# Optimization experiments

Measured on AMD Instinct MI355X. Metric: run time of the kernel, lower is better.

## Reference

```python
import jax, jax.numpy as jnp
import numpy as np
from jax import lax

B = 16
IMG = 384
P = 16
C = 3
DIM = 256
DEPTH = 6
HEADS = 4
DH = 64
INNER = HEADS * DH  # 256
MLP = 512
NC = 21
HP = IMG // P       # 24
N = HP * HP         # 576
PD = C * P * P      # 768
K = 16
SCALE = DH ** -0.5
NEG = -1e9


def _ln(x, g, b):
    mu = x.mean(-1, keepdims=True)
    var = ((x - mu) ** 2).mean(-1, keepdims=True)
    return (x - mu) / jnp.sqrt(var + 1e-5) * g + b


def _conv(x, w, b):
    y = lax.conv_general_dilated(x, w, (1, 1), 'SAME',
                                 dimension_numbers=('NCHW', 'OIHW', 'NCHW'))
    return y + b[None, :, None, None]


def _up2(x):
    b, c, h, w = x.shape
    return jax.image.resize(x, (b, c, 2 * h, 2 * w), 'bilinear')


def _attn(x, g, bt, qkv_w, out_w, out_b, alpha):
    xn = _ln(x, g, bt)
    qkv = xn @ qkv_w                              # [B,N,3*INNER]
    q, k, v = jnp.split(qkv, 3, axis=-1)
    def heads(t):
        return t.reshape(B, N, HEADS, DH).transpose(0, 2, 1, 3)  # b h n d
    q, k, v = heads(q), heads(k), heads(v)
    dots = jnp.einsum('bhid,bhjd->bhij', q, k) * SCALE           # [B,H,N,N]
    vals, idx = lax.top_k(dots, K)                               # [B,H,N,K]
    bi = jnp.arange(B)[:, None, None, None]
    hi = jnp.arange(HEADS)[None, :, None, None]
    ni = jnp.arange(N)[None, None, :, None]
    sparse = jnp.full(dots.shape, NEG, dots.dtype).at[bi, hi, ni, idx].set(vals)
    sparse_attn = jax.nn.softmax(sparse, axis=-1)
    global_attn = jax.nn.softmax(dots, axis=-1)
    a = jnp.clip(alpha, 0.0, 1.0)
    attn = (1 - a) * sparse_attn + a * global_attn
    out = jnp.einsum('bhij,bhjd->bhid', attn, v)                 # [B,H,N,DH]
    out = out.transpose(0, 2, 1, 3).reshape(B, N, INNER)
    return out @ out_w + out_b


def _forward(img, patch_w, patch_b, pos_emb,
             ln1_g, ln1_b, qkv_w, out_w, out_b, alpha,
             ln2_g, ln2_b, ff_w1, ff_b1, ff_w2, ff_b2,
             lnf_g, lnf_b,
             conv1_w, conv1_b, conv2_w, conv2_b, conv3_w, conv3_b):
    # patchify: b c (h p1) (w p2) -> b (h w) (p1 p2 c)
    x = img.reshape(B, C, HP, P, HP, P).transpose(0, 2, 4, 3, 5, 1).reshape(B, N, PD)
    x = x @ patch_w + patch_b + pos_emb
    for i in range(DEPTH):
        x = x + _attn(x, ln1_g[i], ln1_b[i], qkv_w[i], out_w[i], out_b[i], alpha[i])
        h = _ln(x, ln2_g[i], ln2_b[i])
        h = jax.nn.gelu(h @ ff_w1[i] + ff_b1[i], approximate=False)
        x = x + h @ ff_w2[i] + ff_b2[i]
    x = _ln(x, lnf_g, lnf_b)
    x = x.transpose(0, 2, 1).reshape(B, DIM, HP, HP)             # b d h w
    x = jax.nn.relu(_conv(x, conv1_w, conv1_b))
    x = _up2(x)
    x = jax.nn.relu(_conv(x, conv2_w, conv2_b))
    x = _up2(x)
    x = _conv(x, conv3_w, conv3_b)
    return jax.image.resize(x, (B, NC, IMG, IMG), 'bilinear')


def setup_inputs() -> dict:
    key = jax.random.key(0)
    ks = jax.random.split(key, 16)
    s = 0.02
    d = {
        'img': jax.random.normal(ks[0], (B, C, IMG, IMG), jnp.float32),
        'patch_w': jax.random.normal(ks[1], (PD, DIM)) * s,
        'patch_b': jnp.zeros((DIM,)),
        'pos_emb': jax.random.normal(ks[2], (1, N, DIM)) * s,
        'ln1_g': jnp.ones((DEPTH, DIM)), 'ln1_b': jnp.zeros((DEPTH, DIM)),
        'qkv_w': jax.random.normal(ks[3], (DEPTH, DIM, 3 * INNER)) * s,
        'out_w': jax.random.normal(ks[4], (DEPTH, INNER, DIM)) * s,
        'out_b': jnp.zeros((DEPTH, DIM)),
        'alpha': jnp.full((DEPTH,), 0.2),
        'ln2_g': jnp.ones((DEPTH, DIM)), 'ln2_b': jnp.zeros((DEPTH, DIM)),
        'ff_w1': jax.random.normal(ks[5], (DEPTH, DIM, MLP)) * s,
        'ff_b1': jnp.zeros((DEPTH, MLP)),
        'ff_w2': jax.random.normal(ks[6], (DEPTH, MLP, DIM)) * s,
        'ff_b2': jnp.zeros((DEPTH, DIM)),
        'lnf_g': jnp.ones((DIM,)), 'lnf_b': jnp.zeros((DIM,)),
        'conv1_w': jax.random.normal(ks[7], (DIM // 2, DIM, 3, 3)) * s,
        'conv1_b': jnp.zeros((DIM // 2,)),
        'conv2_w': jax.random.normal(ks[8], (DIM // 4, DIM // 2, 3, 3)) * s,
        'conv2_b': jnp.zeros((DIM // 4,)),
        'conv3_w': jax.random.normal(ks[9], (NC, DIM // 4, 1, 1)) * s,
        'conv3_b': jnp.zeros((NC,)),
    }
    return d


def reference(img, patch_w, patch_b, pos_emb,
              ln1_g, ln1_b, qkv_w, out_w, out_b, alpha,
              ln2_g, ln2_b, ff_w1, ff_b1, ff_w2, ff_b2,
              lnf_g, lnf_b,
              conv1_w, conv1_b, conv2_w, conv2_b, conv3_w, conv3_b):
    return _forward(img, patch_w, patch_b, pos_emb,
                    ln1_g, ln1_b, qkv_w, out_w, out_b, alpha,
                    ln2_g, ln2_b, ff_w1, ff_b1, ff_w2, ff_b2,
                    lnf_g, lnf_b,
                    conv1_w, conv1_b, conv2_w, conv2_b, conv3_w, conv3_b)
```

## Files before the change

kernel.cpp:

```cpp
#include <hip/hip_runtime.h>
#include <cfloat>
#include <cmath>

constexpr int NB    = 16;
constexpr int IMGSZ = 384;
constexpr int PSZ   = 16;
constexpr int NCH   = 3;
constexpr int DMODEL= 256;
constexpr int DEPTH = 6;
constexpr int NHEAD = 4;
constexpr int DHEAD = 64;
constexpr int DQKV  = 768;
constexpr int QKS   = 512;
constexpr int DMLP  = 512;
constexpr int NCLS  = 21;
constexpr int HPATCH= 24;
constexpr int NTOK  = 576;
constexpr int NPD   = 768;
constexpr int TOPK  = 16;
constexpr int NROWS = NB * NTOK;
constexpr int OUT_TOTAL = NB * NCLS * IMGSZ * IMGSZ;

constexpr int RPB    = 16;
constexpr int NBLK   = NTOK / RPB;
constexpr int CHUNK  = 64;
constexpr int NCHUNK = NTOK / CHUNK;
constexpr int SCP    = 577;

typedef __attribute__((ext_vector_type(8))) short bf16x8;
typedef __attribute__((ext_vector_type(4))) float f32x4;

__device__ __forceinline__ unsigned short f2bf(float f) {
    unsigned u = __builtin_bit_cast(unsigned, f);
    unsigned r = (u + 0x7FFFu + ((u >> 16) & 1u)) >> 16;
    return (unsigned short)r;
}
__device__ __forceinline__ float bf2f(unsigned short h) {
    unsigned u = ((unsigned)h) << 16;
    return __builtin_bit_cast(float, u);
}

__global__ __launch_bounds__(256) void k_castT(const float* __restrict__ src,
                                               unsigned short* __restrict__ dst,
                                               int K, int N) {
    int t = blockIdx.x * 256 + threadIdx.x;
    if (t >= K * N) return;
    size_t base = (size_t)blockIdx.y * K * N;
    int n = t / K, k = t - n * K;
    dst[base + t] = f2bf(src[base + (size_t)k * N + n]);
}

template <int IC>
__global__ __launch_bounds__(256) void k_castConv(const float* __restrict__ src,
                                                  unsigned short* __restrict__ dst,
                                                  int OC) {
    int t = blockIdx.x * 256 + threadIdx.x;
    if (t >= OC * 9 * IC) return;
    int oc = t / (9 * IC);
    int r = t - oc * 9 * IC;
    int tap = r / IC, ic = r - tap * IC;
    dst[t] = f2bf(src[((size_t)(oc * IC + ic)) * 9 + tap]);
}

__global__ __launch_bounds__(256) void k_patchify(const float* __restrict__ img,
                                                  unsigned short* __restrict__ A) {
    int t = blockIdx.x * 256 + threadIdx.x;
    if (t >= NROWS * NPD) return;
    int r  = t / NPD, pd = t - r * NPD;
    int b  = r / NTOK, n = r - b * NTOK;
    int hy = n / HPATCH, hx = n - hy * HPATCH;
    int c  = pd % NCH;  int q = pd / NCH;
    int p2 = q % PSZ;   int p1 = q / PSZ;
    A[t] = f2bf(img[(((size_t)(b * NCH + c)) * IMGSZ + hy * PSZ + p1) * IMGSZ + hx * PSZ + p2]);
}

template <int BM, int BN, int EPI, int CIN>
__global__ __launch_bounds__(256) void k_mm(
    const unsigned short* __restrict__ Abf,
    const unsigned short* __restrict__ Wt,
    const float* __restrict__ bias,
    float* __restrict__ outf,
    unsigned short* __restrict__ outb,
    unsigned short* __restrict__ outb2,
    unsigned short* __restrict__ vth,
    unsigned short* __restrict__ vtl,
    int M, int Nn, int K, int H, int Wd, int gxd, int gyd)
{
    constexpr int MF = BM / 32;
    constexpr int NF = BN / 32;
    constexpr bool GATHER = (CIN > 0);
    constexpr int AREP = BM * 4 / 256;
    constexpr int BREP = BN * 4 / 256;
    __shared__ __align__(16) short As[4][BM][8];
    __shared__ __align__(16) short Bs[4][BN][8];
    const int tid = threadIdx.x;
    const int p = blockIdx.x;
    const int xr = p & 7, xq = p >> 3;
    const int bm = (xr * (gyd >> 3) + xq / gxd) * BM;
    const int bn = (xq % gxd) * BN;
    const int lane = tid & 63, wid = tid >> 6;
    const int wm = wid >> 1, wn = wid & 1;
    const int l15 = lane & 15, lg = lane >> 4;

    int pb_[AREP], py_[AREP], px_[AREP];
    if (GATHER) {
        #pragma unroll
        for (int rep = 0; rep < AREP; ++rep) {
            int idx = rep * 256 + tid;
            int m = idx >> 2;
            int pix = bm + m;
            px_[rep] = pix % Wd;
            int r = pix / Wd;
            py_[rep] = r % H;
            pb_[rep] = r / H;
        }
    }

    f32x4 acc[MF][NF];
    #pragma unroll
    for (int i = 0; i < MF; ++i)
        #pragma unroll
        for (int j = 0; j < NF; ++j)
            acc[i][j] = (f32x4){0.f, 0.f, 0.f, 0.f};

    for (int k0 = 0; k0 < K; k0 += 32) {
        #pragma unroll
        for (int rep = 0; rep < AREP; ++rep) {
            int idx = rep * 256 + tid;
            int m = idx >> 2, kg = idx & 3;
            if (!GATHER) {
                *(bf16x8*)As[kg][m] =
                    *(const bf16x8*)(Abf + (size_t)(bm + m) * K + k0 + kg * 8);
            } else {
                int k = k0 + kg * 8;
                int tap = k / CIN;
                int ic = k - tap * CIN;
                int dy = tap / 3 - 1, dx = tap % 3 - 1;
                int yy = py_[rep] + dy, xx = px_[rep] + dx;
                bf16x8 v = (bf16x8){0, 0, 0, 0, 0, 0, 0, 0};
                if ((unsigned)yy < (unsigned)H && (unsigned)xx < (unsigned)Wd)
                    v = *(const bf16x8*)(Abf +
                        ((size_t)((pb_[rep] * H + yy) * Wd + xx)) * CIN + ic);
                *(bf16x8*)As[kg][m] = v;
            }
        }
        #pragma unroll
        for (int rep = 0; rep < BREP; ++rep) {
            int idx = rep * 256 + tid;
            int n = idx >> 2, kg = idx & 3;
            *(bf16x8*)Bs[kg][n] =
                *(const bf16x8*)(Wt + (size_t)(bn + n) * K + k0 + kg * 8);
        }
        __syncthreads();
        bf16x8 af[MF], bfv[NF];
        #pragma unroll
        for (int i = 0; i < MF; ++i)
            af[i] = *(const bf16x8*)As[lg][wm * (BM / 2) + i * 16 + l15];
        #pragma unroll
        for (int j = 0; j < NF; ++j)
            bfv[j] = *(const bf16x8*)Bs[lg][wn * (BN / 2) + j * 16 + l15];
        #pragma unroll
        for (int i = 0; i < MF; ++i)
            #pragma unroll
            for (int j = 0; j < NF; ++j)
                acc[i][j] = __builtin_amdgcn_mfma_f32_16x16x32_bf16(
                    af[i], bfv[j], acc[i][j], 0, 0, 0);
        __syncthreads();
    }

    if constexpr (EPI == 8) {
        #pragma unroll
        for (int i = 0; i < MF; ++i) {
            const int row0 = bm + wm * (BM / 2) + i * 16 + lg * 4;
            #pragma unroll
            for (int j = 0; j < NF; ++j) {
                const int col = bn + wn * (BN / 2) + j * 16 + l15;
                if (col < 512) {
                    #pragma unroll
                    for (int r = 0; r < 4; ++r) {
                        float v = acc[i][j][r];
                        unsigned short hi = f2bf(v);
                        outb[(size_t)(row0 + r) * QKS + col] = hi;
                        outb2[(size_t)(row0 + r) * QKS + col] = f2bf(v - bf2f(hi));
                    }
                } else {
                    const int d = col - 512, hh = d >> 6, dd = d & 63;
                    const int bb = row0 / NTOK, n = row0 % NTOK;
                    unsigned long long ph = 0ull, pl = 0ull;
                    #pragma unroll
                    for (int r = 0; r < 4; ++r) {
                        float v = acc[i][j][r];
                        unsigned short hi = f2bf(v);
                        unsigned short lo = f2bf(v - bf2f(hi));
                        ph |= (unsigned long long)hi << (16 * r);
                        pl |= (unsigned long long)lo << (16 * r);
                    }
                    const size_t off = (size_t)((bb * NHEAD + hh) * DHEAD + dd) * NTOK + n;
                    *(unsigned long long*)(vth + off) = ph;
                    *(unsigned long long*)(vtl + off) = pl;
                }
            }
        }
    } else {
        #pragma unroll
        for (int i = 0; i < MF; ++i) {
            const int row0 = bm + wm * (BM / 2) + i * 16 + lg * 4;
            #pragma unroll
            for (int j = 0; j < NF; ++j) {
                const int col = bn + wn * (BN / 2) + j * 16 + l15;
                #pragma unroll
                for (int r = 0; r < 4; ++r) {
                    const int rr = row0 + r;
                    float v = acc[i][j][r] + bias[col];
                    if (EPI == 2) v = 0.5f * v * (1.0f + erff(v * 0.70710678118f));
                    if (EPI == 4) v = fmaxf(v, 0.f);
                    outb[(size_t)rr * Nn + col] = f2bf(v);
                }
            }
        }
    }
}

template <int RES>
__global__ __launch_bounds__(256) void k_gemm_ln(
    const unsigned short* __restrict__ Abf,
    const unsigned short* __restrict__ Wt,
    const float* __restrict__ bias,
    const float* __restrict__ extra,
    const float* __restrict__ lng,
    const float* __restrict__ lnb,
    float* __restrict__ x,
    unsigned short* __restrict__ xn,
    int K, int gyd)
{
    constexpr int BM = 32;
    __shared__ __align__(16) short As[4][BM][8];
    __shared__ __align__(16) short Bs[4][256][8];
    __shared__ float redS[BM][4];
    __shared__ float redQ[BM][4];
    const int tid = threadIdx.x;
    const int p = blockIdx.x;
    const int xr = p & 7, xq = p >> 3;
    const int bm = (xr * (gyd >> 3) + xq) * BM;
    const int lane = tid & 63, wn = tid >> 6;
    const int l15 = lane & 15, lg = lane >> 4;

    f32x4 acc[2][4];
    #pragma unroll
    for (int i = 0; i < 2; ++i)
        #pragma unroll
        for (int j = 0; j < 4; ++j)
            acc[i][j] = (f32x4){0.f, 0.f, 0.f, 0.f};

    for (int k0 = 0; k0 < K; k0 += 32) {
        if (tid < BM * 4) {
            int m = tid >> 2, kg = tid & 3;
            *(bf16x8*)As[kg][m] = *(const bf16x8*)(Abf + (size_t)(bm + m) * K + k0 + kg * 8);
        }
        #pragma unroll
        for (int rep = 0; rep < 4; ++rep) {
            int idx = rep * 256 + tid;
            int n = idx >> 2, kg = idx & 3;
            *(bf16x8*)Bs[kg][n] = *(const bf16x8*)(Wt + (size_t)n * K + k0 + kg * 8);
        }
        __syncthreads();
        bf16x8 af[2], bfv[4];
        #pragma unroll
        for (int i = 0; i < 2; ++i)
            af[i] = *(const bf16x8*)As[lg][i * 16 + l15];
        #pragma unroll
        for (int j = 0; j < 4; ++j)
            bfv[j] = *(const bf16x8*)Bs[lg][wn * 64 + j * 16 + l15];
        #pragma unroll
        for (int i = 0; i < 2; ++i)
            #pragma unroll
            for (int j = 0; j < 4; ++j)
                acc[i][j] = __builtin_amdgcn_mfma_f32_16x16x32_bf16(
                    af[i], bfv[j], acc[i][j], 0, 0, 0);
        __syncthreads();
    }

    #pragma unroll
    for (int i = 0; i < 2; ++i) {
        #pragma unroll
        for (int j = 0; j < 4; ++j) {
            const int col = wn * 64 + j * 16 + l15;
            #pragma unroll
            for (int r = 0; r < 4; ++r) {
                const int rr = bm + i * 16 + lg * 4 + r;
                float v = acc[i][j][r] + bias[col];
                if (RES) v += x[(size_t)rr * DMODEL + col];
                else     v += extra[(size_t)(rr % NTOK) * DMODEL + col];
                x[(size_t)rr * DMODEL + col] = v;
                acc[i][j][r] = v;
            }
        }
    }
    float s[2][4];
    #pragma unroll
    for (int i = 0; i < 2; ++i)
        #pragma unroll
        for (int r = 0; r < 4; ++r)
            s[i][r] = ((acc[i][0][r] + acc[i][1][r]) + acc[i][2][r]) + acc[i][3][r];
    #pragma unroll
    for (int off = 1; off < 16; off <<= 1)
        #pragma unroll
        for (int i = 0; i < 2; ++i)
            #pragma unroll
            for (int r = 0; r < 4; ++r)
                s[i][r] += __shfl_xor(s[i][r], off);
    if (l15 == 0)
        #pragma unroll
        for (int i = 0; i < 2; ++i)
            #pragma unroll
            for (int r = 0; r < 4; ++r)
                redS[i * 16 + lg * 4 + r][wn] = s[i][r];
    __syncthreads();
    float mu[2][4];
    #pragma unroll
    for (int i = 0; i < 2; ++i)
        #pragma unroll
        for (int r = 0; r < 4; ++r) {
            const float* q = redS[i * 16 + lg * 4 + r];
            mu[i][r] = (((q[0] + q[1]) + q[2]) + q[3]) * (1.0f / DMODEL);
        }
    float qq[2][4];
    #pragma unroll
    for (int i = 0; i < 2; ++i)
        #pragma unroll
        for (int r = 0; r < 4; ++r) {
            float d0 = acc[i][0][r] - mu[i][r], d1 = acc[i][1][r] - mu[i][r];
            float d2 = acc[i][2][r] - mu[i][r], d3 = acc[i][3][r] - mu[i][r];
            qq[i][r] = ((d0 * d0 + d1 * d1) + d2 * d2) + d3 * d3;
        }
    #pragma unroll
    for (int off = 1; off < 16; off <<= 1)
        #pragma unroll
        for (int i = 0; i < 2; ++i)
            #pragma unroll
            for (int r = 0; r < 4; ++r)
                qq[i][r] += __shfl_xor(qq[i][r], off);
    if (l15 == 0)
        #pragma unroll
        for (int i = 0; i < 2; ++i)
            #pragma unroll
            for (int r = 0; r < 4; ++r)
                redQ[i * 16 + lg * 4 + r][wn] = qq[i][r];
    __syncthreads();
    #pragma unroll
    for (int i = 0; i < 2; ++i) {
        #pragma unroll
        for (int r = 0; r < 4; ++r) {
            const float* q = redQ[i * 16 + lg * 4 + r];
            float var = (((q[0] + q[1]) + q[2]) + q[3]) * (1.0f / DMODEL);
            float rstd = rsqrtf(var + 1e-5f);
            const int rr = bm + i * 16 + lg * 4 + r;
            #pragma unroll
            for (int j = 0; j < 4; ++j) {
                const int col = wn * 64 + j * 16 + l15;
                float o = (acc[i][j][r] - mu[i][r]) * rstd * lng[col] + lnb[col];
                xn[(size_t)rr * DMODEL + col] = f2bf(o);
            }
        }
    }
}

struct KF { bf16x8 h0, h1, l0, l1; };
__device__ __forceinline__ KF ldkf(const unsigned short* __restrict__ hi,
                                   const unsigned short* __restrict__ lo,
                                   size_t off) {
    KF f;
    f.h0 = *(const bf16x8*)(hi + off);
    f.h1 = *(const bf16x8*)(hi + off + 32);
    f.l0 = *(const bf16x8*)(lo + off);
    f.l1 = *(const bf16x8*)(lo + off + 32);
    return f;
}

__global__ __launch_bounds__(256, 4) void k_attn(
    const unsigned short* __restrict__ qhi,
    const unsigned short* __restrict__ qlo,
    const unsigned short* __restrict__ vthi,
    const unsigned short* __restrict__ vtlo,
    const float* __restrict__ alpha_l,
    unsigned short* __restrict__ ao) {
    __shared__ __align__(16) unsigned char ub[16 * SCP * 4];
    float* scp = (float*)ub;
    short* pj  = (short*)ub;

    const int tid = threadIdx.x;
    const int lane = tid & 63;
    const int ct = tid >> 6;
    const int l15 = lane & 15, lg = lane >> 4;
    const int xr = blockIdx.x & 7, xq = blockIdx.x >> 3;
    const int g = xr + 8 * (xq / NBLK);
    const int b = g >> 2, h = g & 3;
    const int i0 = (xq % NBLK) * RPB;

    bf16x8 aqh0, aqh1, aql0, aql1;
    {
        const size_t qoff = (size_t)(b * NTOK + i0 + l15) * QKS + h * DHEAD + lg * 8;
        aqh0 = *(const bf16x8*)(qhi + qoff);
        aqh1 = *(const bf16x8*)(qhi + qoff + 32);
        aql0 = *(const bf16x8*)(qlo + qoff);
        aql1 = *(const bf16x8*)(qlo + qoff + 32);
    }

    const size_t kRow = (size_t)(b * NTOK + ct * 16 + l15) * QKS + DMODEL + h * DHEAD + lg * 8;
    KF kc = ldkf(qhi, qlo, kRow);
    #pragma unroll
    for (int c = 0; c < NCHUNK; ++c) {
        KF kn;
        if (c + 1 < NCHUNK)
            kn = ldkf(qhi, qlo, kRow + (size_t)(c + 1) * CHUNK * QKS);
        f32x4 sD = (f32x4){0.f, 0.f, 0.f, 0.f};
        sD = __builtin_amdgcn_mfma_f32_16x16x32_bf16(aqh0, kc.h0, sD, 0, 0, 0);
        sD = __builtin_amdgcn_mfma_f32_16x16x32_bf16(aqh0, kc.l0, sD, 0, 0, 0);
        sD = __builtin_amdgcn_mfma_f32_16x16x32_bf16(aql0, kc.h0, sD, 0, 0, 0);
        sD = __builtin_amdgcn_mfma_f32_16x16x32_bf16(aqh1, kc.h1, sD, 0, 0, 0);
        sD = __builtin_amdgcn_mfma_f32_16x16x32_bf16(aqh1, kc.l1, sD, 0, 0, 0);
        sD = __builtin_amdgcn_mfma_f32_16x16x32_bf16(aql1, kc.h1, sD, 0, 0, 0);
        const int col = c * CHUNK + ct * 16 + l15;
        #pragma unroll
        for (int r = 0; r < 4; ++r)
            scp[(lg * 4 + r) * SCP + col] = sD[r] * 0.125f;
        if (c + 1 < NCHUNK) kc = kn;
    }
    __syncthreads();

    float o_[4][9];
    const int wrow = ct * 4;
    #pragma unroll
    for (int rr = 0; rr < 4; ++rr)
        #pragma unroll
        for (int t = 0; t < 9; ++t)
            o_[rr][t] = scp[(wrow + rr) * SCP + t * 64 + lane];
    __syncthreads();

    unsigned msk[4] = {0u, 0u, 0u, 0u};
    float M_[4];
    for (int k = 0; k < TOPK; ++k) {
        float lm[4];
        #pragma unroll
        for (int rr = 0; rr < 4; ++rr) {
            float m0 = -FLT_MAX;
            #pragma unroll
            for (int t = 0; t < 9; ++t) {
                float v = ((msk[rr] >> t) & 1u) ? -FLT_MAX : o_[rr][t];
                m0 = fmaxf(m0, v);
            }
            lm[rr] = m0;
        }
        #pragma unroll
        for (int off = 1; off < 64; off <<= 1) {
            #pragma unroll
            for (int rr = 0; rr < 4; ++rr)
                lm[rr] = fmaxf(lm[rr], __shfl_xor(lm[rr], off));
        }
        if (k == 0) {
            #pragma unroll
            for (int rr = 0; rr < 4; ++rr) M_[rr] = lm[rr];
        }
        #pragma unroll
        for (int rr = 0; rr < 4; ++rr) {
            int js = -1;
            #pragma unroll
            for (int t = 0; t < 9; ++t) {
                if (js < 0) {
                    unsigned long long bal =
                        __ballot((((msk[rr] >> t) & 1u) == 0u) && (o_[rr][t] == lm[rr]));
                    if (bal) js = t * 64 + (int)__builtin_ctzll(bal);
                }
            }
            if ((js & 63) == lane) msk[rr] |= 1u << (js >> 6);
        }
    }

    const float al = fminf(fmaxf(alpha_l[0], 0.f), 1.f);
    float gs[4], ss[4];
    #pragma unroll
    for (int rr = 0; rr < 4; ++rr) {
        float g_ = 0.f, s_ = 0.f;
        #pragma unroll
        for (int t = 0; t < 9; ++t) {
            float e = __expf(o_[rr][t] - M_[rr]);
            g_ += e;
            if ((msk[rr] >> t) & 1u) s_ += e;
        }
        gs[rr] = g_; ss[rr] = s_;
    }
    #pragma unroll
    for (int off = 1; off < 64; off <<= 1) {
        #pragma unroll
        for (int rr = 0; rr < 4; ++rr) {
            gs[rr] += __shfl_xor(gs[rr], off);
            ss[rr] += __shfl_xor(ss[rr], off);
        }
    }
    float ca[4], cs[4];
    #pragma unroll
    for (int rr = 0; rr < 4; ++rr) {
        ca[rr] = al / gs[rr];
        cs[rr] = (1.f - al) / ss[rr];
    }

    const size_t vRow = (size_t)((b * NHEAD + h) * DHEAD + ct * 16 + l15) * NTOK + lg * 8;
    KF vc = ldkf(vthi, vtlo, vRow);
    f32x4 acc = (f32x4){0.f, 0.f, 0.f, 0.f};
    #pragma unroll
    for (int c = 0; c < NCHUNK; ++c) {
        KF vn;
        if (c + 1 < NCHUNK)
            vn = ldkf(vthi, vtlo, vRow + (size_t)(c + 1) * CHUNK);
        short* pb = pj + (c & 1) * (2 * 16 * 72);
        #pragma unroll
        for (int rr = 0; rr < 4; ++rr) {
            float e = __expf(o_[rr][c] - M_[rr]);
            float wv = e * (ca[rr] + (((msk[rr] >> c) & 1u) ? cs[rr] : 0.f));
            unsigned short hi = f2bf(wv);
            pb[(wrow + rr) * 72 + lane] = (short)hi;
            pb[16 * 72 + (wrow + rr) * 72 + lane] = (short)f2bf(wv - bf2f(hi));
        }
        __syncthreads();
        const short* pr = pb + l15 * 72 + lg * 8;
        bf16x8 ah0 = *(const bf16x8*)(pr);
        bf16x8 ah1 = *(const bf16x8*)(pr + 32);
        bf16x8 al0 = *(const bf16x8*)(pr + 16 * 72);
        bf16x8 al1 = *(const bf16x8*)(pr + 16 * 72 + 32);
        acc = __builtin_amdgcn_mfma_f32_16x16x32_bf16(ah0, vc.h0, acc, 0, 0, 0);
        acc = __builtin_amdgcn_mfma_f32_16x16x32_bf16(ah0, vc.l0, acc, 0, 0, 0);
        acc = __builtin_amdgcn_mfma_f32_16x16x32_bf16(al0, vc.h0, acc, 0, 0, 0);
        acc = __builtin_amdgcn_mfma_f32_16x16x32_bf16(ah1, vc.h1, acc, 0, 0, 0);
        acc = __builtin_amdgcn_mfma_f32_16x16x32_bf16(ah1, vc.l1, acc, 0, 0, 0);
        acc = __builtin_amdgcn_mfma_f32_16x16x32_bf16(al1, vc.h1, acc, 0, 0, 0);
        if (c + 1 < NCHUNK) vc = vn;
    }
    {
        const int qrow = i0 + lg * 4;
        const int dcol = h * DHEAD + ct * 16 + l15;
        #pragma unroll
        for (int r = 0; r < 4; ++r)
            ao[(size_t)(b * NTOK + qrow + r) * DMODEL + dcol] = f2bf(acc[r]);
    }
}

__device__ __forceinline__ void bilin_axis(float sF, int H, int& i0, int& i1, float& f) {
    float fl = floorf(sF);
    f = sF - fl;
    int lo = (int)fl;
    i0 = lo < 0 ? 0 : (lo > H - 1 ? H - 1 : lo);
    int hi = lo + 1;
    i1 = hi < 0 ? 0 : (hi > H - 1 ? H - 1 : hi);
}

__global__ __launch_bounds__(256) void k_up2n(const unsigned short* __restrict__ in,
                                              unsigned short* __restrict__ outp,
                                              int Hin, int C) {
    const int Ho = 2 * Hin;
    const int CG = C / 8;
    const int total = NB * Ho * Ho * CG;
    int t = blockIdx.x * 256 + threadIdx.x;
    if (t >= total) return;
    int cg = t % CG; int r = t / CG;
    int x = r % Ho; r /= Ho;
    int y = r % Ho; int b = r / Ho;
    int i0, i1, j0, j1; float fy, fx;
    bilin_axis(0.5f * y - 0.25f, Hin, i0, i1, fy);
    bilin_axis(0.5f * x - 0.25f, Hin, j0, j1, fx);
    const unsigned short* base = in + (size_t)b * Hin * Hin * C + cg * 8;
    const bf16x8 p00 = *(const bf16x8*)(base + (size_t)(i0 * Hin + j0) * C);
    const bf16x8 p01 = *(const bf16x8*)(base + (size_t)(i0 * Hin + j1) * C);
    const bf16x8 p10 = *(const bf16x8*)(base + (size_t)(i1 * Hin + j0) * C);
    const bf16x8 p11 = *(const bf16x8*)(base + (size_t)(i1 * Hin + j1) * C);
    bf16x8 o;
    #pragma unroll
    for (int e = 0; e < 8; ++e) {
        float v = (1.f - fy) * ((1.f - fx) * bf2f((unsigned short)p00[e]) + fx * bf2f((unsigned short)p01[e]))
                + fy        * ((1.f - fx) * bf2f((unsigned short)p10[e]) + fx * bf2f((unsigned short)p11[e]));
        o[e] = (short)f2bf(v);
    }
    *(bf16x8*)(outp + (size_t)t * 8) = o;
}

__global__ __launch_bounds__(256) void k_conv3n(const unsigned short* __restrict__ in,
                                                const float* __restrict__ w,
                                                const float* __restrict__ bias,
                                                float* __restrict__ outp) {
    __shared__ float ws_[NCLS * 64];
    for (int i = threadIdx.x; i < NCLS * 64; i += 256) ws_[i] = w[i];
    __syncthreads();
    int t = blockIdx.x * 256 + threadIdx.x;
    if (t >= NB * 9216) return;
    int pix = t % 9216, b = t / 9216;
    float xv[64];
    const unsigned short* p = in + (size_t)t * 64;
    #pragma unroll
    for (int c = 0; c < 8; ++c) {
        bf16x8 v = *(const bf16x8*)(p + c * 8);
        #pragma unroll
        for (int e = 0; e < 8; ++e) xv[c * 8 + e] = bf2f((unsigned short)v[e]);
    }
    float* op = outp + (size_t)b * NCLS * 9216 + pix;
    #pragma unroll
    for (int o = 0; o < NCLS; ++o) {
        float acc = bias[o];
        #pragma unroll
        for (int ic = 0; ic < 64; ++ic) acc += ws_[o * 64 + ic] * xv[ic];
        op[(size_t)o * 9216] = acc;
    }
}

__global__ __launch_bounds__(256) void k_resize4(const float* __restrict__ in,
                                                 float* __restrict__ outp) {
    int t = blockIdx.x * 256 + threadIdx.x;
    if (t >= OUT_TOTAL) return;
    int x = t % IMGSZ; int r = t / IMGSZ; int y = r % IMGSZ; int bc = r / IMGSZ;
    int i0, i1, j0, j1; float fy, fx;
    bilin_axis(0.25f * y - 0.375f, 96, i0, i1, fy);
    bilin_axis(0.25f * x - 0.375f, 96, j0, j1, fx);
    const float* p = in + (size_t)bc * 9216;
    outp[t] = (1.f - fy) * ((1.f - fx) * p[i0 * 96 + j0] + fx * p[i0 * 96 + j1])
            + fy        * ((1.f - fx) * p[i1 * 96 + j0] + fx * p[i1 * 96 + j1]);
}

extern "C" void kernel_launch(void* const* d_in, const int* in_sizes, int n_in,
                              void* d_out, int out_size, void* d_ws, size_t ws_size,
                              hipStream_t stream) {
    const float* img     = (const float*)d_in[0];
    const float* patch_w = (const float*)d_in[1];
    const float* patch_b = (const float*)d_in[2];
    const float* pos_emb = (const float*)d_in[3];
    const float* ln1_g   = (const float*)d_in[4];
    const float* ln1_b   = (const float*)d_in[5];
    const float* qkv_w   = (const float*)d_in[6];
    const float* out_w   = (const float*)d_in[7];
    const float* out_b   = (const float*)d_in[8];
    const float* alpha   = (const float*)d_in[9];
    const float* ln2_g   = (const float*)d_in[10];
    const float* ln2_b   = (const float*)d_in[11];
    const float* ff_w1   = (const float*)d_in[12];
    const float* ff_b1   = (const float*)d_in[13];
    const float* ff_w2   = (const float*)d_in[14];
    const float* ff_b2   = (const float*)d_in[15];
    const float* lnf_g   = (const float*)d_in[16];
    const float* lnf_b   = (const float*)d_in[17];
    const float* conv1_w = (const float*)d_in[18];
    const float* conv1_b = (const float*)d_in[19];
    const float* conv2_w = (const float*)d_in[20];
    const float* conv2_b = (const float*)d_in[21];
    const float* conv3_w = (const float*)d_in[22];
    const float* conv3_b = (const float*)d_in[23];

    float* x = (float*)d_ws;
    unsigned short* qkv_hi = (unsigned short*)(x + (size_t)NROWS * DMODEL);
    unsigned short* qkv_lo = qkv_hi + (size_t)NROWS * QKS;
    unsigned short* xn_bf  = qkv_lo + (size_t)NROWS * QKS;
    unsigned short* ao_bf  = xn_bf + (size_t)NROWS * DMODEL;
    unsigned short* h_bf   = ao_bf + (size_t)NROWS * DMODEL;
    unsigned short* pA     = h_bf + (size_t)NROWS * DMLP;
    unsigned short* wts    = pA + (size_t)NROWS * NPD;
    unsigned short* pwt  = wts;
    unsigned short* qwt  = pwt  + 768 * 256;
    unsigned short* owt  = qwt  + 6 * 768 * 256;
    unsigned short* f1wt = owt  + 6 * 256 * 256;
    unsigned short* f2wt = f1wt + 6 * 256 * 512;
    unsigned short* c1wt = f2wt + 6 * 512 * 256;
    unsigned short* c2wt = c1wt + 128 * 9 * 256;
    unsigned short* vthi = c2wt + 64 * 9 * 128;
    unsigned short* vtlo = vthi + (size_t)64 * 64 * NTOK;
    unsigned short* c1n = ao_bf;
    unsigned short* u1n = h_bf;
    unsigned short* c2n = xn_bf;
    unsigned short* u2n = qkv_hi;
    float* c3 = (float*)pA;

    k_castT<<<dim3(768, 1), 256, 0, stream>>>(patch_w, pwt, NPD, DMODEL);
    k_castT<<<dim3(768, 6), 256, 0, stream>>>(qkv_w, qwt, DMODEL, DQKV);
    k_castT<<<dim3(256, 6), 256, 0, stream>>>(out_w, owt, DMODEL, DMODEL);
    k_castT<<<dim3(512, 6), 256, 0, stream>>>(ff_w1, f1wt, DMODEL, DMLP);
    k_castT<<<dim3(512, 6), 256, 0, stream>>>(ff_w2, f2wt, DMLP, DMODEL);
    k_castConv<256><<<1152, 256, 0, stream>>>(conv1_w, c1wt, 128);
    k_castConv<128><<<288, 256, 0, stream>>>(conv2_w, c2wt, 64);

    k_patchify<<<(NROWS * NPD + 255) / 256, 256, 0, stream>>>(img, pA);
    k_gemm_ln<0><<<288, 256, 0, stream>>>(
        pA, pwt, patch_b, pos_emb, ln1_g, ln1_b, x, xn_bf, NPD, 288);

    for (int l = 0; l < DEPTH; ++l) {
        k_mm<128, 128, 8, 0><<<6 * 72, 256, 0, stream>>>(
            xn_bf, qwt + (size_t)l * DQKV * DMODEL, nullptr,
            nullptr, qkv_hi, qkv_lo, vthi, vtlo,
            NROWS, DQKV, DMODEL, 0, 0, 6, 72);
        k_attn<<<NBLK * NHEAD * NB, 256, 0, stream>>>(
            qkv_hi, qkv_lo, vthi, vtlo, alpha + l, ao_bf);
        k_gemm_ln<1><<<288, 256, 0, stream>>>(
            ao_bf, owt + (size_t)l * DMODEL * DMODEL, out_b + l * DMODEL, nullptr,
            ln2_g + l * DMODEL, ln2_b + l * DMODEL, x, xn_bf, DMODEL, 288);
        k_mm<128, 128, 2, 0><<<4 * 72, 256, 0, stream>>>(
            xn_bf, f1wt + (size_t)l * DMLP * DMODEL, ff_b1 + l * DMLP,
            nullptr, h_bf, nullptr, nullptr, nullptr,
            NROWS, DMLP, DMODEL, 0, 0, 4, 72);
        const float* ng = (l + 1 < DEPTH) ? (ln1_g + (l + 1) * DMODEL) : lnf_g;
        const float* nb = (l + 1 < DEPTH) ? (ln1_b + (l + 1) * DMODEL) : lnf_b;
        k_gemm_ln<1><<<288, 256, 0, stream>>>(
            h_bf, f2wt + (size_t)l * DMODEL * DMLP, ff_b2 + l * DMODEL, nullptr,
            ng, nb, x, xn_bf, DMLP, 288);
    }

    k_mm<64, 128, 4, 256><<<1 * 144, 256, 0, stream>>>(
        xn_bf, c1wt, conv1_b, nullptr, c1n, nullptr, nullptr, nullptr,
        NROWS, 128, 9 * 256, 24, 24, 1, 144);
    k_up2n<<<(NB * 48 * 48 * 16 + 255) / 256, 256, 0, stream>>>(c1n, u1n, 24, 128);
    k_mm<128, 64, 4, 128><<<1 * 288, 256, 0, stream>>>(
        u1n, c2wt, conv2_b, nullptr, c2n, nullptr, nullptr, nullptr,
        NB * 48 * 48, 64, 9 * 128, 48, 48, 1, 288);
    k_up2n<<<(NB * 96 * 96 * 8 + 255) / 256, 256, 0, stream>>>(c2n, u2n, 48, 64);
    k_conv3n<<<(NB * 9216 + 255) / 256, 256, 0, stream>>>(u2n, conv3_w, conv3_b, c3);
    k_resize4<<<(OUT_TOTAL + 255) / 256, 256, 0, stream>>>(c3, (float*)d_out);
}
```

Before: 1.368 ms.

## Double attention block to 512 threads, splitting chunks across two wave groups

The attention kernel now launches 8 waves per block instead of 4. The two wave groups alternate over key and value chunks for the QK and PV MFMAs. Each wave owns 2 query rows instead of 4 for the top-k and softmax phase, which halves the serial per-wave work. The two partial PV accumulators are then summed through shared memory. The cost is the loss of software prefetch of the next K/V chunk, an extra reduction and sync, and higher register and occupancy pressure from launch_bounds(512,8). The reduction buffer at offset 16384 must fit inside the shared buffer.

```diff
diff --git a/kernel.cpp b/kernel.cpp
--- a/kernel.cpp
+++ b/kernel.cpp
@@ -377,7 +377,7 @@
     return f;
 }
 
-__global__ __launch_bounds__(256, 4) void k_attn(
+__global__ __launch_bounds__(512, 8) void k_attn(
     const unsigned short* __restrict__ qhi,
     const unsigned short* __restrict__ qlo,
     const unsigned short* __restrict__ vthi,
@@ -387,10 +387,13 @@
     __shared__ __align__(16) unsigned char ub[16 * SCP * 4];
     float* scp = (float*)ub;
     short* pj  = (short*)ub;
+    float* red = (float*)(ub + 16384);
 
     const int tid = threadIdx.x;
     const int lane = tid & 63;
-    const int ct = tid >> 6;
+    const int w = tid >> 6;
+    const int par = w >> 2;
+    const int ct = w & 3;
     const int l15 = lane & 15, lg = lane >> 4;
     const int xr = blockIdx.x & 7, xq = blockIdx.x >> 3;
     const int g = xr + 8 * (xq / NBLK);
@@ -407,12 +410,8 @@
     }
 
     const size_t kRow = (size_t)(b * NTOK + ct * 16 + l15) * QKS + DMODEL + h * DHEAD + lg * 8;
-    KF kc = ldkf(qhi, qlo, kRow);
-    #pragma unroll
-    for (int c = 0; c < NCHUNK; ++c) {
-        KF kn;
-        if (c + 1 < NCHUNK)
-            kn = ldkf(qhi, qlo, kRow + (size_t)(c + 1) * CHUNK * QKS);
+    for (int c = par; c < NCHUNK; c += 2) {
+        KF kc = ldkf(qhi, qlo, kRow + (size_t)c * CHUNK * QKS);
         f32x4 sD = (f32x4){0.f, 0.f, 0.f, 0.f};
         sD = __builtin_amdgcn_mfma_f32_16x16x32_bf16(aqh0, kc.h0, sD, 0, 0, 0);
         sD = __builtin_amdgcn_mfma_f32_16x16x32_bf16(aqh0, kc.l0, sD, 0, 0, 0);
@@ -424,25 +423,24 @@
         #pragma unroll
         for (int r = 0; r < 4; ++r)
             scp[(lg * 4 + r) * SCP + col] = sD[r] * 0.125f;
-        if (c + 1 < NCHUNK) kc = kn;
     }
     __syncthreads();
 
-    float o_[4][9];
-    const int wrow = ct * 4;
-    #pragma unroll
-    for (int rr = 0; rr < 4; ++rr)
+    float o_[2][9];
+    const int r0 = 2 * w;
+    #pragma unroll
+    for (int rr = 0; rr < 2; ++rr)
         #pragma unroll
         for (int t = 0; t < 9; ++t)
-            o_[rr][t] = scp[(wrow + rr) * SCP + t * 64 + lane];
+            o_[rr][t] = scp[(r0 + rr) * SCP + t * 64 + lane];
     __syncthreads();
 
-    unsigned msk[4] = {0u, 0u, 0u, 0u};
-    float M_[4];
+    unsigned msk[2] = {0u, 0u};
+    float M_[2];
     for (int k = 0; k < TOPK; ++k) {
-        float lm[4];
-        #pragma unroll
-        for (int rr = 0; rr < 4; ++rr) {
+        float lm[2];
+        #pragma unroll
+        for (int rr = 0; rr < 2; ++rr) {
             float m0 = -FLT_MAX;
             #pragma unroll
             for (int t = 0; t < 9; ++t) {
@@ -454,15 +452,15 @@
         #pragma unroll
         for (int off = 1; off < 64; off <<= 1) {
             #pragma unroll
-            for (int rr = 0; rr < 4; ++rr)
+            for (int rr = 0; rr < 2; ++rr)
                 lm[rr] = fmaxf(lm[rr], __shfl_xor(lm[rr], off));
         }
         if (k == 0) {
             #pragma unroll
-            for (int rr = 0; rr < 4; ++rr) M_[rr] = lm[rr];
-        }
-        #pragma unroll
-        for (int rr = 0; rr < 4; ++rr) {
+            for (int rr = 0; rr < 2; ++rr) M_[rr] = lm[rr];
+        }
+        #pragma unroll
+        for (int rr = 0; rr < 2; ++rr) {
             int js = -1;
             #pragma unroll
             for (int t = 0; t < 9; ++t) {
@@ -477,9 +475,9 @@
     }
 
     const float al = fminf(fmaxf(alpha_l[0], 0.f), 1.f);
-    float gs[4], ss[4];
-    #pragma unroll
-    for (int rr = 0; rr < 4; ++rr) {
+    float gs[2], ss[2];
+    #pragma unroll
+    for (int rr = 0; rr < 2; ++rr) {
         float g_ = 0.f, s_ = 0.f;
         #pragma unroll
         for (int t = 0; t < 9; ++t) {
@@ -492,55 +490,60 @@
     #pragma unroll
     for (int off = 1; off < 64; off <<= 1) {
         #pragma unroll
-        for (int rr = 0; rr < 4; ++rr) {
+        for (int rr = 0; rr < 2; ++rr) {
             gs[rr] += __shfl_xor(gs[rr], off);
             ss[rr] += __shfl_xor(ss[rr], off);
         }
     }
-    float ca[4], cs[4];
-    #pragma unroll
-    for (int rr = 0; rr < 4; ++rr) {
+    float ca[2], cs[2];
+    #pragma unroll
+    for (int rr = 0; rr < 2; ++rr) {
         ca[rr] = al / gs[rr];
         cs[rr] = (1.f - al) / ss[rr];
     }
 
     const size_t vRow = (size_t)((b * NHEAD + h) * DHEAD + ct * 16 + l15) * NTOK + lg * 8;
-    KF vc = ldkf(vthi, vtlo, vRow);
     f32x4 acc = (f32x4){0.f, 0.f, 0.f, 0.f};
-    #pragma unroll
     for (int c = 0; c < NCHUNK; ++c) {
-        KF vn;
-        if (c + 1 < NCHUNK)
-            vn = ldkf(vthi, vtlo, vRow + (size_t)(c + 1) * CHUNK);
         short* pb = pj + (c & 1) * (2 * 16 * 72);
         #pragma unroll
-        for (int rr = 0; rr < 4; ++rr) {
+        for (int rr = 0; rr < 2; ++rr) {
             float e = __expf(o_[rr][c] - M_[rr]);
             float wv = e * (ca[rr] + (((msk[rr] >> c) & 1u) ? cs[rr] : 0.f));
             unsigned short hi = f2bf(wv);
-            pb[(wrow + rr) * 72 + lane] = (short)hi;
-            pb[16 * 72 + (wrow + rr) * 72 + lane] = (short)f2bf(wv - bf2f(hi));
+            pb[(r0 + rr) * 72 + lane] = (short)hi;
+            pb[16 * 72 + (r0 + rr) * 72 + lane] = (short)f2bf(wv - bf2f(hi));
         }
         __syncthreads();
-        const short* pr = pb + l15 * 72 + lg * 8;
-        bf16x8 ah0 = *(const bf16x8*)(pr);
-        bf16x8 ah1 = *(const bf16x8*)(pr + 32);
-        bf16x8 al0 = *(const bf16x8*)(pr + 16 * 72);
-        bf16x8 al1 = *(const bf16x8*)(pr + 16 * 72 + 32);
-        acc = __builtin_amdgcn_mfma_f32_16x16x32_bf16(ah0, vc.h0, acc, 0, 0, 0);
-        acc = __builtin_amdgcn_mfma_f32_16x16x32_bf16(ah0, vc.l0, acc, 0, 0, 0);
-        acc = __builtin_amdgcn_mfma_f32_16x16x32_bf16(al0, vc.h0, acc, 0, 0, 0);
-        acc = __builtin_amdgcn_mfma_f32_16x16x32_bf16(ah1, vc.h1, acc, 0, 0, 0);
-        acc = __builtin_amdgcn_mfma_f32_16x16x32_bf16(ah1, vc.l1, acc, 0, 0, 0);
-        acc = __builtin_amdgcn_mfma_f32_16x16x32_bf16(al1, vc.h1, acc, 0, 0, 0);
-        if (c + 1 < NCHUNK) vc = vn;
-    }
-    {
+        if ((c & 1) == par) {
+            KF vc = ldkf(vthi, vtlo, vRow + (size_t)c * CHUNK);
+            const short* pr = pb + l15 * 72 + lg * 8;
+            bf16x8 ah0 = *(const bf16x8*)(pr);
+            bf16x8 ah1 = *(const bf16x8*)(pr + 32);
+            bf16x8 al0 = *(const bf16x8*)(pr + 16 * 72);
+            bf16x8 al1 = *(const bf16x8*)(pr + 16 * 72 + 32);
+            acc = __builtin_amdgcn_mfma_f32_16x16x32_bf16(ah0, vc.h0, acc, 0, 0, 0);
+            acc = __builtin_amdgcn_mfma_f32_16x16x32_bf16(ah0, vc.l0, acc, 0, 0, 0);
+            acc = __builtin_amdgcn_mfma_f32_16x16x32_bf16(al0, vc.h0, acc, 0, 0, 0);
+            acc = __builtin_amdgcn_mfma_f32_16x16x32_bf16(ah1, vc.h1, acc, 0, 0, 0);
+            acc = __builtin_amdgcn_mfma_f32_16x16x32_bf16(ah1, vc.l1, acc, 0, 0, 0);
+            acc = __builtin_amdgcn_mfma_f32_16x16x32_bf16(al1, vc.h1, acc, 0, 0, 0);
+        }
+    }
+    if (par == 1) {
+        #pragma unroll
+        for (int r = 0; r < 4; ++r)
+            red[(ct * 16 + l15) * 17 + lg * 4 + r] = acc[r];
+    }
+    __syncthreads();
+    if (par == 0) {
         const int qrow = i0 + lg * 4;
         const int dcol = h * DHEAD + ct * 16 + l15;
         #pragma unroll
-        for (int r = 0; r < 4; ++r)
-            ao[(size_t)(b * NTOK + qrow + r) * DMODEL + dcol] = f2bf(acc[r]);
+        for (int r = 0; r < 4; ++r) {
+            float v = acc[r] + red[(ct * 16 + l15) * 17 + lg * 4 + r];
+            ao[(size_t)(b * NTOK + qrow + r) * DMODEL + dcol] = f2bf(v);
+        }
     }
 }
 
@@ -691,7 +694,7 @@
             xn_bf, qwt + (size_t)l * DQKV * DMODEL, nullptr,
             nullptr, qkv_hi, qkv_lo, vthi, vtlo,
             NROWS, DQKV, DMODEL, 0, 0, 6, 72);
-        k_attn<<<NBLK * NHEAD * NB, 256, 0, stream>>>(
+        k_attn<<<NBLK * NHEAD * NB, 512, 0, stream>>>(
             qkv_hi, qkv_lo, vthi, vtlo, alpha + l, ao_bf);
         k_gemm_ln<1><<<288, 256, 0, stream>>>(
             ao_bf, owt + (size_t)l * DMODEL * DMODEL, out_b + l * DMODEL, nullptr,
```

Result: faster. 1.306 ms (-4.6%).
